# Kernel tuning notes

Hardware: AMD Instinct MI355X
Metric: run time of the kernel (lower is better)

## Reference

```python
import jax, jax.numpy as jnp
import numpy as np

N, E, L, D = 4, 64, 512, 768


def setup_inputs() -> dict:
    key = jax.random.key(0)
    k1, k2, k3, k4 = jax.random.split(key, 4)
    doc_state = jax.random.normal(k1, (N, L, D), dtype=jnp.float32)
    # 0/1 entity membership mask, float as in the torch module's multiply
    entity_mapping = jax.random.randint(k2, (N, E, L), 0, 2).astype(jnp.float32)
    # lens consistent with the mask; clamp to >=1 to avoid divide-by-zero
    entity_lens = jnp.maximum(entity_mapping.sum(axis=-1), 1.0)
    W = jax.random.normal(k3, (D, 2 * D), dtype=jnp.float32) * 0.02  # torch Linear weight [out, in]
    b = jnp.zeros((D,), dtype=jnp.float32)
    return {"doc_state": doc_state, "entity_mapping": entity_mapping,
            "entity_lens": entity_lens, "W": W, "b": b}


def reference(doc_state, entity_mapping, entity_lens, W, b):
    # entity_states: N x E x L x d (the large broadcast intermediate)
    entity_states = entity_mapping[:, :, :, None] * doc_state[:, None, :, :]
    max_pooled = jnp.max(entity_states, axis=2)                      # N x E x d
    mean_pooled = jnp.sum(entity_states, axis=2) / entity_lens[:, :, None]  # N x E x d
    output = jnp.concatenate([max_pooled, mean_pooled], axis=2)      # N x E x 2d
    return jnp.einsum('nek,dk->ned', output, W) + b                  # N x E x d
```

## Files before the change

### kernel.cpp

```cpp
#include <hip/hip_runtime.h>
#include <hip/hip_bf16.h>
#include <math.h>

#define PN 4
#define PE 64
#define PL 512
#define PD 768
#define PK2 (2 * PD)
#define PM (PN * PE)

#define EG 4
#define DCW 128
#define NDC (PD / DCW)
#define NPOOLB (PN * (PE / EG) * NDC)
#define NCVT ((PD * PK2) / (512 * 8))

using bf16x8 = __attribute__((ext_vector_type(8))) short;
using f32x4  = __attribute__((ext_vector_type(4))) float;

static __device__ __forceinline__ unsigned short f2bf(float x) {
    unsigned int u = __float_as_uint(x);
    unsigned int r = (u + 0x7FFFu + ((u >> 16) & 1u)) >> 16;
    return (unsigned short)r;
}

__global__ __launch_bounds__(512) void pool_full(
    const float* __restrict__ doc,
    const float* __restrict__ map,
    const float* __restrict__ lens,
    const float* __restrict__ W,
    unsigned short* __restrict__ Pb,
    unsigned short* __restrict__ Wb)
{
    const int bid = blockIdx.x;
    const int tid = threadIdx.x;

    if (bid >= NPOOLB) {
        const size_t i = ((size_t)(bid - NPOOLB) * 512 + tid) * 8;
        const float4 a = *reinterpret_cast<const float4*>(W + i);
        const float4 c = *reinterpret_cast<const float4*>(W + i + 4);
        union { unsigned short s[8]; uint4 v; } r;
        r.s[0] = f2bf(a.x); r.s[1] = f2bf(a.y); r.s[2] = f2bf(a.z); r.s[3] = f2bf(a.w);
        r.s[4] = f2bf(c.x); r.s[5] = f2bf(c.y); r.s[6] = f2bf(c.z); r.s[7] = f2bf(c.w);
        *reinterpret_cast<uint4*>(Wb + i) = r.v;
        return;
    }

    __shared__ float2 lmax[8][EG][64];
    __shared__ float2 lsum[8][EG][64];

    const int dc   = bid % NDC;
    const int rest = bid / NDC;
    const int eg   = rest & 15;
    const int n    = rest >> 4;
    const int e0   = eg * EG;
    const int d0   = dc * DCW;
    const int w    = tid >> 6;
    const int lane = tid & 63;

    unsigned long long mk[EG];
    #pragma unroll
    for (int e = 0; e < EG; ++e) {
        const float m = map[((size_t)n * PE + e0 + e) * PL + w * 64 + lane];
        mk[e] = __ballot(m != 0.0f);
    }

    const float2* docp = reinterpret_cast<const float2*>(
        doc + ((size_t)n * PL + w * 64) * PD + d0) + lane;

    float2 mx[EG], sm[EG];
    #pragma unroll
    for (int e = 0; e < EG; ++e) {
        mx[e] = make_float2(-INFINITY, -INFINITY);
        sm[e] = make_float2(0.f, 0.f);
    }

    #pragma unroll 8
    for (int l = 0; l < 64; ++l) {
        const float2 v = docp[(size_t)l * (PD / 2)];
        #pragma unroll
        for (int e = 0; e < EG; ++e) {
            const bool bit = (mk[e] >> l) & 1ull;
            const float cx = bit ? v.x : 0.0f;
            const float cy = bit ? v.y : 0.0f;
            sm[e].x += cx;  sm[e].y += cy;
            mx[e].x = fmaxf(mx[e].x, cx);
            mx[e].y = fmaxf(mx[e].y, cy);
        }
    }

    #pragma unroll
    for (int e = 0; e < EG; ++e) {
        lmax[w][e][lane] = mx[e];
        lsum[w][e][lane] = sm[e];
    }
    __syncthreads();

    const int slot = tid & 255;
    const int e  = slot >> 6;
    const int ln = slot & 63;
    const int ne = n * PE + e0 + e;
    if (tid < 256) {
        float2 m = lmax[0][e][ln];
        #pragma unroll
        for (int ww = 1; ww < 8; ++ww) {
            const float2 t = lmax[ww][e][ln];
            m.x = fmaxf(m.x, t.x);
            m.y = fmaxf(m.y, t.y);
        }
        const unsigned int pk = (unsigned int)f2bf(m.x) | ((unsigned int)f2bf(m.y) << 16);
        *reinterpret_cast<unsigned int*>(Pb + (size_t)ne * PK2 + d0 + ln * 2) = pk;
    } else {
        float2 s = lsum[0][e][ln];
        #pragma unroll
        for (int ww = 1; ww < 8; ++ww) {
            const float2 t = lsum[ww][e][ln];
            s.x += t.x;
            s.y += t.y;
        }
        const float inv = 1.0f / lens[ne];
        const unsigned int pk = (unsigned int)f2bf(s.x * inv) | ((unsigned int)f2bf(s.y * inv) << 16);
        *reinterpret_cast<unsigned int*>(Pb + (size_t)ne * PK2 + PD + d0 + ln * 2) = pk;
    }
}

__global__ __launch_bounds__(64) void gemm_mfma1(
    const unsigned short* __restrict__ Pb,
    const unsigned short* __restrict__ Wb,
    const float* __restrict__ b,
    float* __restrict__ out)
{
    const int lane = threadIdx.x;
    const int tile = blockIdx.x;
    const int rt = tile & 15;
    const int ct = tile >> 4;
    const int r0 = rt * 16, d0 = ct * 16;

    const int fr = lane & 15;
    const int kg = lane >> 4;

    const unsigned short* pA = Pb + (size_t)(r0 + fr) * PK2 + kg * 8;
    const unsigned short* pB = Wb + (size_t)(d0 + fr) * PK2 + kg * 8;

    f32x4 acc = {0.f, 0.f, 0.f, 0.f};
    #pragma unroll 8
    for (int k0 = 0; k0 < PK2; k0 += 32) {
        const bf16x8 a  = *reinterpret_cast<const bf16x8*>(pA + k0);
        const bf16x8 bb = *reinterpret_cast<const bf16x8*>(pB + k0);
        acc = __builtin_amdgcn_mfma_f32_16x16x32_bf16(a, bb, acc, 0, 0, 0);
    }

    const int c = d0 + fr;
    const float bias = b[c];
    #pragma unroll
    for (int j = 0; j < 4; ++j)
        out[(size_t)(r0 + kg * 4 + j) * PD + c] = acc[j] + bias;
}

__global__ __launch_bounds__(256) void fused_kernel(
    const float* __restrict__ doc, const float* __restrict__ map,
    const float* __restrict__ lens, const float* __restrict__ W,
    const float* __restrict__ b, float* __restrict__ out)
{
    __shared__ float Prow[PK2];
    const int ne = blockIdx.x, n = ne >> 6, t = threadIdx.x;
    const float* docn = doc + (size_t)n * PL * PD;
    const float* mrow = map + (size_t)ne * PL;
    float mx0=-INFINITY, mx1=-INFINITY, mx2=-INFINITY, s0=0.f, s1=0.f, s2=0.f;
    bool has_zero = false;
    for (int l = 0; l < PL; ++l) {
        const float m = mrow[l];
        if (m != 0.0f) {
            const float* dr = docn + (size_t)l * PD;
            const float a = dr[t], c = dr[t+256], e = dr[t+512];
            mx0=fmaxf(mx0,a); s0+=a; mx1=fmaxf(mx1,c); s1+=c; mx2=fmaxf(mx2,e); s2+=e;
        } else has_zero = true;
    }
    if (has_zero) { mx0=fmaxf(mx0,0.f); mx1=fmaxf(mx1,0.f); mx2=fmaxf(mx2,0.f); }
    const float invlen = 1.0f / lens[ne];
    Prow[t]=mx0; Prow[t+256]=mx1; Prow[t+512]=mx2;
    Prow[PD+t]=s0*invlen; Prow[PD+t+256]=s1*invlen; Prow[PD+t+512]=s2*invlen;
    __syncthreads();
    #pragma unroll
    for (int i = 0; i < 3; ++i) {
        const int d = t + i*256;
        const float* wrow = W + (size_t)d * PK2;
        float acc = 0.f;
        for (int k = 0; k < PK2; k += 4) {
            const float4 w = *reinterpret_cast<const float4*>(&wrow[k]);
            acc += Prow[k]*w.x + Prow[k+1]*w.y + Prow[k+2]*w.z + Prow[k+3]*w.w;
        }
        out[(size_t)ne * PD + d] = acc + b[d];
    }
}

extern "C" void kernel_launch(void* const* d_in, const int* in_sizes, int n_in,
                              void* d_out, int out_size, void* d_ws, size_t ws_size,
                              hipStream_t stream) {
    const float* doc  = (const float*)d_in[0];
    const float* map  = (const float*)d_in[1];
    const float* lens = (const float*)d_in[2];
    const float* W    = (const float*)d_in[3];
    const float* b    = (const float*)d_in[4];
    float* out = (float*)d_out;

    const size_t pb_bytes = (size_t)PM * PK2 * sizeof(unsigned short);
    const size_t wb_bytes = (size_t)PD * PK2 * sizeof(unsigned short);
    const size_t need     = pb_bytes + wb_bytes;

    if (ws_size >= need) {
        unsigned short* Pb = (unsigned short*)d_ws;
        unsigned short* Wb = (unsigned short*)((char*)d_ws + pb_bytes);
        pool_full<<<dim3(NPOOLB + NCVT), dim3(512), 0, stream>>>(
            doc, map, lens, W, Pb, Wb);
        gemm_mfma1<<<dim3((PM / 16) * (PD / 16)), dim3(64), 0, stream>>>(Pb, Wb, b, out);
    } else {
        fused_kernel<<<dim3(PM), dim3(256), 0, stream>>>(doc, map, lens, W, b, out);
    }
}
```

Baseline: 30.44 us.

## Fuse pooling and GEMM into one cooperative kernel with grid sync and split-K

Merges the pooling/W-conversion kernel and the MFMA GEMM into a single cooperative launch of 384 blocks, using a grid-wide sync between the phases. This removes the second kernel launch and its gap. The W conversion is folded into the first 288 blocks rather than running in extra blocks. The GEMM phase runs two 16x16 tiles per block, with four waves each doing a quarter of K, reduced through shared memory. The cost is a grid barrier, extra conversion work on some pool blocks, and a fallback to the old two-kernel path if the cooperative launch fails.

```diff
diff --git a/kernel.cpp b/kernel.cpp
--- a/kernel.cpp
+++ b/kernel.cpp
@@ -1,6 +1,9 @@
 #include <hip/hip_runtime.h>
 #include <hip/hip_bf16.h>
+#include <hip/hip_cooperative_groups.h>
 #include <math.h>
+
+namespace cg = cooperative_groups;
 
 #define PN 4
 #define PE 64
@@ -12,8 +15,8 @@
 #define EG 4
 #define DCW 128
 #define NDC (PD / DCW)
-#define NPOOLB (PN * (PE / EG) * NDC)
-#define NCVT ((PD * PK2) / (512 * 8))
+#define NBLK (PN * (PE / EG) * NDC)
+#define CVTB 288
 
 using bf16x8 = __attribute__((ext_vector_type(8))) short;
 using f32x4  = __attribute__((ext_vector_type(4))) float;
@@ -24,13 +27,157 @@
     return (unsigned short)r;
 }
 
-__global__ __launch_bounds__(512) void pool_full(
+__global__ __launch_bounds__(512) void fused_coop(
     const float* __restrict__ doc,
     const float* __restrict__ map,
     const float* __restrict__ lens,
     const float* __restrict__ W,
+    const float* __restrict__ b,
     unsigned short* __restrict__ Pb,
-    unsigned short* __restrict__ Wb)
+    unsigned short* __restrict__ Wb,
+    float* __restrict__ out)
+{
+    __shared__ union {
+        struct { float2 lmax[8][EG][64]; float2 lsum[8][EG][64]; } pool;
+        f32x4 racc[8][64];
+    } sh;
+
+    const int bid  = blockIdx.x;
+    const int tid  = threadIdx.x;
+    const int w    = tid >> 6;
+    const int lane = tid & 63;
+
+    if (bid < CVTB) {
+        const size_t i = ((size_t)bid * 512 + tid) * 8;
+        const float4 a = *reinterpret_cast<const float4*>(W + i);
+        const float4 c = *reinterpret_cast<const float4*>(W + i + 4);
+        union { unsigned short s[8]; uint4 v; } r;
+        r.s[0] = f2bf(a.x); r.s[1] = f2bf(a.y); r.s[2] = f2bf(a.z); r.s[3] = f2bf(a.w);
+        r.s[4] = f2bf(c.x); r.s[5] = f2bf(c.y); r.s[6] = f2bf(c.z); r.s[7] = f2bf(c.w);
+        *reinterpret_cast<uint4*>(Wb + i) = r.v;
+    }
+
+    {
+        const int dc   = bid % NDC;
+        const int rest = bid / NDC;
+        const int eg   = rest & 15;
+        const int n    = rest >> 4;
+        const int e0   = eg * EG;
+        const int d0   = dc * DCW;
+
+        unsigned long long mk[EG];
+        #pragma unroll
+        for (int e = 0; e < EG; ++e) {
+            const float m = map[((size_t)n * PE + e0 + e) * PL + w * 64 + lane];
+            mk[e] = __ballot(m != 0.0f);
+        }
+
+        const float2* docp = reinterpret_cast<const float2*>(
+            doc + ((size_t)n * PL + w * 64) * PD + d0) + lane;
+
+        float2 mx[EG], sm[EG];
+        #pragma unroll
+        for (int e = 0; e < EG; ++e) {
+            mx[e] = make_float2(-INFINITY, -INFINITY);
+            sm[e] = make_float2(0.f, 0.f);
+        }
+
+        #pragma unroll 8
+        for (int l = 0; l < 64; ++l) {
+            const float2 v = docp[(size_t)l * (PD / 2)];
+            #pragma unroll
+            for (int e = 0; e < EG; ++e) {
+                const bool bit = (mk[e] >> l) & 1ull;
+                const float cx = bit ? v.x : 0.0f;
+                const float cy = bit ? v.y : 0.0f;
+                sm[e].x += cx;  sm[e].y += cy;
+                mx[e].x = fmaxf(mx[e].x, cx);
+                mx[e].y = fmaxf(mx[e].y, cy);
+            }
+        }
+
+        #pragma unroll
+        for (int e = 0; e < EG; ++e) {
+            sh.pool.lmax[w][e][lane] = mx[e];
+            sh.pool.lsum[w][e][lane] = sm[e];
+        }
+        __syncthreads();
+
+        const int slot = tid & 255;
+        const int e  = slot >> 6;
+        const int ln = slot & 63;
+        const int ne = n * PE + e0 + e;
+        if (tid < 256) {
+            float2 m = sh.pool.lmax[0][e][ln];
+            #pragma unroll
+            for (int ww = 1; ww < 8; ++ww) {
+                const float2 t = sh.pool.lmax[ww][e][ln];
+                m.x = fmaxf(m.x, t.x);
+                m.y = fmaxf(m.y, t.y);
+            }
+            const unsigned int pk = (unsigned int)f2bf(m.x) | ((unsigned int)f2bf(m.y) << 16);
+            *reinterpret_cast<unsigned int*>(Pb + (size_t)ne * PK2 + d0 + ln * 2) = pk;
+        } else {
+            float2 s = sh.pool.lsum[0][e][ln];
+            #pragma unroll
+            for (int ww = 1; ww < 8; ++ww) {
+                const float2 t = sh.pool.lsum[ww][e][ln];
+                s.x += t.x;
+                s.y += t.y;
+            }
+            const float inv = 1.0f / lens[ne];
+            const unsigned int pk = (unsigned int)f2bf(s.x * inv) | ((unsigned int)f2bf(s.y * inv) << 16);
+            *reinterpret_cast<unsigned int*>(Pb + (size_t)ne * PK2 + PD + d0 + ln * 2) = pk;
+        }
+    }
+
+    cg::this_grid().sync();
+
+    {
+        const int tile = bid * 2 + (w >> 2);
+        const int kq   = w & 3;
+        const int rt = tile & 15;
+        const int ct = tile >> 4;
+        const int r0 = rt * 16, d0 = ct * 16;
+
+        const int fr = lane & 15;
+        const int kg = lane >> 4;
+
+        const unsigned short* pA = Pb + (size_t)(r0 + fr) * PK2 + kq * 384 + kg * 8;
+        const unsigned short* pB = Wb + (size_t)(d0 + fr) * PK2 + kq * 384 + kg * 8;
+
+        f32x4 acc = {0.f, 0.f, 0.f, 0.f};
+        #pragma unroll
+        for (int k0 = 0; k0 < 384; k0 += 32) {
+            const bf16x8 a  = *reinterpret_cast<const bf16x8*>(pA + k0);
+            const bf16x8 bb = *reinterpret_cast<const bf16x8*>(pB + k0);
+            acc = __builtin_amdgcn_mfma_f32_16x16x32_bf16(a, bb, acc, 0, 0, 0);
+        }
+
+        sh.racc[w][lane] = acc;
+        __syncthreads();
+
+        if ((w & 3) == 0) {
+            f32x4 a = sh.racc[w][lane];
+            a += sh.racc[w + 1][lane];
+            a += sh.racc[w + 2][lane];
+            a += sh.racc[w + 3][lane];
+            const int c = d0 + fr;
+            const float bias = b[c];
+            #pragma unroll
+            for (int j = 0; j < 4; ++j)
+                out[(size_t)(r0 + kg * 4 + j) * PD + c] = a[j] + bias;
+        }
+    }
+}
+
+#define NPOOLB NBLK
+#define NCVT ((PD * PK2) / (512 * 8))
+
+__global__ __launch_bounds__(512) void pool_full(
+    const float* __restrict__ doc, const float* __restrict__ map,
+    const float* __restrict__ lens, const float* __restrict__ W,
+    unsigned short* __restrict__ Pb, unsigned short* __restrict__ Wb)
 {
     const int bid = blockIdx.x;
     const int tid = threadIdx.x;
@@ -125,23 +272,16 @@
 }
 
 __global__ __launch_bounds__(64) void gemm_mfma1(
-    const unsigned short* __restrict__ Pb,
-    const unsigned short* __restrict__ Wb,
-    const float* __restrict__ b,
-    float* __restrict__ out)
+    const unsigned short* __restrict__ Pb, const unsigned short* __restrict__ Wb,
+    const float* __restrict__ b, float* __restrict__ out)
 {
     const int lane = threadIdx.x;
     const int tile = blockIdx.x;
-    const int rt = tile & 15;
-    const int ct = tile >> 4;
+    const int rt = tile & 15, ct = tile >> 4;
     const int r0 = rt * 16, d0 = ct * 16;
-
-    const int fr = lane & 15;
-    const int kg = lane >> 4;
-
+    const int fr = lane & 15, kg = lane >> 4;
     const unsigned short* pA = Pb + (size_t)(r0 + fr) * PK2 + kg * 8;
     const unsigned short* pB = Wb + (size_t)(d0 + fr) * PK2 + kg * 8;
-
     f32x4 acc = {0.f, 0.f, 0.f, 0.f};
     #pragma unroll 8
     for (int k0 = 0; k0 < PK2; k0 += 32) {
@@ -149,7 +289,6 @@
         const bf16x8 bb = *reinterpret_cast<const bf16x8*>(pB + k0);
         acc = __builtin_amdgcn_mfma_f32_16x16x32_bf16(a, bb, acc, 0, 0, 0);
     }
-
     const int c = d0 + fr;
     const float bias = b[c];
     #pragma unroll
@@ -211,6 +350,16 @@
     if (ws_size >= need) {
         unsigned short* Pb = (unsigned short*)d_ws;
         unsigned short* Wb = (unsigned short*)((char*)d_ws + pb_bytes);
+
+        void* args[] = {
+            (void*)&doc, (void*)&map, (void*)&lens, (void*)&W, (void*)&b,
+            (void*)&Pb, (void*)&Wb, (void*)&out
+        };
+        hipError_t err = hipLaunchCooperativeKernel(
+            (const void*)fused_coop, dim3(NBLK), dim3(512), args, 0, stream);
+        if (err == hipSuccess) return;
+        (void)hipGetLastError();
+
         pool_full<<<dim3(NPOOLB + NCVT), dim3(512), 0, stream>>>(
             doc, map, lens, W, Pb, Wb);
         gemm_mfma1<<<dim3((PM / 16) * (PD / 16)), dim3(64), 0, stream>>>(Pb, Wb, b, out);
```

After: 89.87 us. +195.3%, slower.

## Narrow pooling columns per block and split GEMM K across two waves

Applied to the files above, without the earlier changes.

The pooling kernel now handles 64-wide column chunks with scalar float loads instead of 128-wide float2 chunks, doubling the pool block count to fill more CUs. The masked select becomes a multiply by a 0/1 factor. The GEMM kernel splits the K dimension across two waves with two independent MFMA accumulator chains each, then reduces through shared memory. The aim is more parallelism and less MFMA dependency latency, at the cost of narrower memory accesses, 16-bit scattered stores and an extra block-level sync.

```diff
diff --git a/kernel.cpp b/kernel.cpp
--- a/kernel.cpp
+++ b/kernel.cpp
@@ -10,10 +10,10 @@
 #define PM (PN * PE)
 
 #define EG 4
-#define DCW 128
+#define DCW 64
 #define NDC (PD / DCW)
 #define NPOOLB (PN * (PE / EG) * NDC)
-#define NCVT ((PD * PK2) / (512 * 8))
+#define NCVT 288
 
 using bf16x8 = __attribute__((ext_vector_type(8))) short;
 using f32x4  = __attribute__((ext_vector_type(4))) float;
@@ -24,7 +24,7 @@
     return (unsigned short)r;
 }
 
-__global__ __launch_bounds__(512) void pool_full(
+__global__ __launch_bounds__(512) void pool_v5(
     const float* __restrict__ doc,
     const float* __restrict__ map,
     const float* __restrict__ lens,
@@ -46,8 +46,8 @@
         return;
     }
 
-    __shared__ float2 lmax[8][EG][64];
-    __shared__ float2 lsum[8][EG][64];
+    __shared__ float lmax[8][EG][64];
+    __shared__ float lsum[8][EG][64];
 
     const int dc   = bid % NDC;
     const int rest = bid / NDC;
@@ -65,27 +65,21 @@
         mk[e] = __ballot(m != 0.0f);
     }
 
-    const float2* docp = reinterpret_cast<const float2*>(
-        doc + ((size_t)n * PL + w * 64) * PD + d0) + lane;
-
-    float2 mx[EG], sm[EG];
-    #pragma unroll
-    for (int e = 0; e < EG; ++e) {
-        mx[e] = make_float2(-INFINITY, -INFINITY);
-        sm[e] = make_float2(0.f, 0.f);
-    }
-
-    #pragma unroll 8
+    const float* docp = doc + ((size_t)n * PL + w * 64) * PD + d0 + lane;
+
+    float mx[EG], sm[EG];
+    #pragma unroll
+    for (int e = 0; e < EG; ++e) { mx[e] = -INFINITY; sm[e] = 0.f; }
+
+    #pragma unroll 16
     for (int l = 0; l < 64; ++l) {
-        const float2 v = docp[(size_t)l * (PD / 2)];
+        const float v = docp[(size_t)l * PD];
         #pragma unroll
         for (int e = 0; e < EG; ++e) {
-            const bool bit = (mk[e] >> l) & 1ull;
-            const float cx = bit ? v.x : 0.0f;
-            const float cy = bit ? v.y : 0.0f;
-            sm[e].x += cx;  sm[e].y += cy;
-            mx[e].x = fmaxf(mx[e].x, cx);
-            mx[e].y = fmaxf(mx[e].y, cy);
+            const float mval = ((mk[e] >> l) & 1ull) ? 1.0f : 0.0f;
+            const float cand = mval * v;
+            sm[e] += cand;
+            mx[e] = fmaxf(mx[e], cand);
         }
     }
 
@@ -100,37 +94,30 @@
     const int e  = slot >> 6;
     const int ln = slot & 63;
     const int ne = n * PE + e0 + e;
+    const int d  = d0 + ln;
     if (tid < 256) {
-        float2 m = lmax[0][e][ln];
-        #pragma unroll
-        for (int ww = 1; ww < 8; ++ww) {
-            const float2 t = lmax[ww][e][ln];
-            m.x = fmaxf(m.x, t.x);
-            m.y = fmaxf(m.y, t.y);
-        }
-        const unsigned int pk = (unsigned int)f2bf(m.x) | ((unsigned int)f2bf(m.y) << 16);
-        *reinterpret_cast<unsigned int*>(Pb + (size_t)ne * PK2 + d0 + ln * 2) = pk;
+        float m = lmax[0][e][ln];
+        #pragma unroll
+        for (int ww = 1; ww < 8; ++ww) m = fmaxf(m, lmax[ww][e][ln]);
+        Pb[(size_t)ne * PK2 + d] = f2bf(m);
     } else {
-        float2 s = lsum[0][e][ln];
-        #pragma unroll
-        for (int ww = 1; ww < 8; ++ww) {
-            const float2 t = lsum[ww][e][ln];
-            s.x += t.x;
-            s.y += t.y;
-        }
-        const float inv = 1.0f / lens[ne];
-        const unsigned int pk = (unsigned int)f2bf(s.x * inv) | ((unsigned int)f2bf(s.y * inv) << 16);
-        *reinterpret_cast<unsigned int*>(Pb + (size_t)ne * PK2 + PD + d0 + ln * 2) = pk;
-    }
-}
-
-__global__ __launch_bounds__(64) void gemm_mfma1(
+        float s = lsum[0][e][ln];
+        #pragma unroll
+        for (int ww = 1; ww < 8; ++ww) s += lsum[ww][e][ln];
+        Pb[(size_t)ne * PK2 + PD + d] = f2bf(s * (1.0f / lens[ne]));
+    }
+}
+
+__global__ __launch_bounds__(128) void gemm_ks2(
     const unsigned short* __restrict__ Pb,
     const unsigned short* __restrict__ Wb,
     const float* __restrict__ b,
     float* __restrict__ out)
 {
-    const int lane = threadIdx.x;
+    __shared__ f32x4 red[64];
+
+    const int w    = threadIdx.x >> 6;
+    const int lane = threadIdx.x & 63;
     const int tile = blockIdx.x;
     const int rt = tile & 15;
     const int ct = tile >> 4;
@@ -138,23 +125,34 @@
 
     const int fr = lane & 15;
     const int kg = lane >> 4;
-
-    const unsigned short* pA = Pb + (size_t)(r0 + fr) * PK2 + kg * 8;
-    const unsigned short* pB = Wb + (size_t)(d0 + fr) * PK2 + kg * 8;
-
-    f32x4 acc = {0.f, 0.f, 0.f, 0.f};
-    #pragma unroll 8
-    for (int k0 = 0; k0 < PK2; k0 += 32) {
-        const bf16x8 a  = *reinterpret_cast<const bf16x8*>(pA + k0);
-        const bf16x8 bb = *reinterpret_cast<const bf16x8*>(pB + k0);
-        acc = __builtin_amdgcn_mfma_f32_16x16x32_bf16(a, bb, acc, 0, 0, 0);
-    }
-
-    const int c = d0 + fr;
-    const float bias = b[c];
-    #pragma unroll
-    for (int j = 0; j < 4; ++j)
-        out[(size_t)(r0 + kg * 4 + j) * PD + c] = acc[j] + bias;
+    const int kb = w * (PK2 / 2);
+
+    const unsigned short* pA = Pb + (size_t)(r0 + fr) * PK2 + kb + kg * 8;
+    const unsigned short* pB = Wb + (size_t)(d0 + fr) * PK2 + kb + kg * 8;
+
+    f32x4 acc0 = {0.f, 0.f, 0.f, 0.f};
+    f32x4 acc1 = {0.f, 0.f, 0.f, 0.f};
+    #pragma unroll
+    for (int k0 = 0; k0 < PK2 / 2; k0 += 64) {
+        const bf16x8 a0 = *reinterpret_cast<const bf16x8*>(pA + k0);
+        const bf16x8 b0 = *reinterpret_cast<const bf16x8*>(pB + k0);
+        acc0 = __builtin_amdgcn_mfma_f32_16x16x32_bf16(a0, b0, acc0, 0, 0, 0);
+        const bf16x8 a1 = *reinterpret_cast<const bf16x8*>(pA + k0 + 32);
+        const bf16x8 b1 = *reinterpret_cast<const bf16x8*>(pB + k0 + 32);
+        acc1 = __builtin_amdgcn_mfma_f32_16x16x32_bf16(a1, b1, acc1, 0, 0, 0);
+    }
+    f32x4 acc = acc0 + acc1;
+
+    if (w == 1) red[lane] = acc;
+    __syncthreads();
+    if (w == 0) {
+        acc += red[lane];
+        const int c = d0 + fr;
+        const float bias = b[c];
+        #pragma unroll
+        for (int j = 0; j < 4; ++j)
+            out[(size_t)(r0 + kg * 4 + j) * PD + c] = acc[j] + bias;
+    }
 }
 
 __global__ __launch_bounds__(256) void fused_kernel(
@@ -211,9 +209,9 @@
     if (ws_size >= need) {
         unsigned short* Pb = (unsigned short*)d_ws;
         unsigned short* Wb = (unsigned short*)((char*)d_ws + pb_bytes);
-        pool_full<<<dim3(NPOOLB + NCVT), dim3(512), 0, stream>>>(
+        pool_v5<<<dim3(NPOOLB + NCVT), dim3(512), 0, stream>>>(
             doc, map, lens, W, Pb, Wb);
-        gemm_mfma1<<<dim3((PM / 16) * (PD / 16)), dim3(64), 0, stream>>>(Pb, Wb, b, out);
+        gemm_ks2<<<dim3((PM / 16) * (PD / 16)), dim3(128), 0, stream>>>(Pb, Wb, b, out);
     } else {
         fused_kernel<<<dim3(PM), dim3(256), 0, stream>>>(doc, map, lens, W, b, out);
     }
```

Measured after the change: 30.47 us. Within noise of the previous version (+0.1%).
